# Kernel optimization log

Measured on AMD Instinct MI355X. Metric: run time of the kernel, lower is better.

The kernel has to match this reference:

```python
import jax, jax.numpy as jnp
import numpy as np

N_NODES = 100000
N_EDGES = 800000
NODE_DIM = 128
HIDDEN = 256
OUT_DIM = 512
N_LAYERS = 4
N_GRAPHS = 64


def _linear_init(key, out_f, in_f):
    kw, kb = jax.random.split(key)
    bound = 1.0 / np.sqrt(in_f)
    w = jax.random.uniform(kw, (out_f, in_f), jnp.float32, -bound, bound)
    b = jax.random.uniform(kb, (out_f,), jnp.float32, -bound, bound)
    return w, b


def setup_inputs() -> dict:
    key = jax.random.key(0)
    ks = jax.random.split(key, 16)
    x = jax.random.normal(ks[0], (N_NODES, NODE_DIM), jnp.float32)
    edge_index = jax.random.randint(ks[1], (2, N_EDGES), 0, N_NODES, jnp.int64)
    batch = jnp.sort(jax.random.randint(ks[2], (N_NODES,), 0, N_GRAPHS, jnp.int64))
    node_w, node_b = _linear_init(ks[3], HIDDEN, NODE_DIM)
    gw1, gb1, gw2, gb2 = [], [], [], []
    for i in range(N_LAYERS):
        w1, b1 = _linear_init(ks[4 + 2 * i], HIDDEN, HIDDEN)
        w2, b2 = _linear_init(ks[5 + 2 * i], HIDDEN, HIDDEN)
        gw1.append(w1); gb1.append(b1); gw2.append(w2); gb2.append(b2)
    gin_w1 = jnp.stack(gw1); gin_b1 = jnp.stack(gb1)
    gin_w2 = jnp.stack(gw2); gin_b2 = jnp.stack(gb2)
    eps = jnp.zeros((N_LAYERS,), jnp.float32)  # train_eps init 0
    out_w1, out_b1 = _linear_init(ks[12], HIDDEN, HIDDEN)
    out_w2, out_b2 = _linear_init(ks[13], OUT_DIM, HIDDEN)
    return {
        "x": x, "edge_index": edge_index, "batch": batch,
        "node_w": node_w, "node_b": node_b,
        "gin_w1": gin_w1, "gin_b1": gin_b1,
        "gin_w2": gin_w2, "gin_b2": gin_b2, "eps": eps,
        "out_w1": out_w1, "out_b1": out_b1,
        "out_w2": out_w2, "out_b2": out_b2,
    }


def reference(x, edge_index, batch, node_w, node_b, gin_w1, gin_b1, gin_w2,
              gin_b2, eps, out_w1, out_b1, out_w2, out_b2):
    src, dst = edge_index[0], edge_index[1]
    # node projection + relu
    h = jax.nn.relu(x @ node_w.T + node_b)  # [N, H]
    for i in range(N_LAYERS):
        # GINConv: mlp((1+eps)*x + sum_{j in N(i)} x_j); x_j = h[src], agg at dst
        agg = jax.ops.segment_sum(h[src], dst, num_segments=N_NODES)
        z = (1.0 + eps[i]) * h + agg
        z = jax.nn.relu(z @ gin_w1[i].T + gin_b1[i])
        z = z @ gin_w2[i].T + gin_b2[i]
        h = jax.nn.relu(z)  # outer relu in forward
    # global_mean_pool over batch assignment
    counts = jax.ops.segment_sum(jnp.ones((N_NODES,), h.dtype), batch,
                                 num_segments=N_GRAPHS)
    sums = jax.ops.segment_sum(h, batch, num_segments=N_GRAPHS)
    h_graph = sums / jnp.maximum(counts, 1.0)[:, None]  # [B, H]
    out = jax.nn.relu(h_graph @ out_w1.T + out_b1) @ out_w2.T + out_b2
    return out  # [B, OUT_DIM]
```

## Files before the change

kernel.cpp:

```cpp
#include <hip/hip_runtime.h>
#include <stdint.h>

#define N_NODES   100000
#define N_EDGES   800000
#define NODE_DIM  128
#define HIDDEN    256
#define OUT_DIM   512
#define N_LAYERS  4
#define N_GRAPHS  64
#define POOL_CHUNKS 8
#define SCAN_BLK  1024
#define SCAN_NB   ((N_NODES + SCAN_BLK - 1) / SCAN_BLK)

typedef _Float16 f16;
typedef __attribute__((ext_vector_type(8)))  _Float16 f16x8;
typedef __attribute__((ext_vector_type(4)))  _Float16 f16x4;
typedef __attribute__((ext_vector_type(4)))  float    f32x4;
typedef __attribute__((ext_vector_type(16))) float    f32x16;

__global__ void k_f2h(const float* __restrict__ in, f16* __restrict__ out, int n4) {
    int i = blockIdx.x * 256 + threadIdx.x;
    if (i < n4) {
        f32x4 v = *(const f32x4*)(in + (size_t)i * 4);
        f16x4 o;
        o[0] = (f16)v[0]; o[1] = (f16)v[1]; o[2] = (f16)v[2]; o[3] = (f16)v[3];
        *(f16x4*)(out + (size_t)i * 4) = o;
    }
}

__global__ void k_hist(const int* __restrict__ ei, int* __restrict__ deg) {
    int e = blockIdx.x * 256 + threadIdx.x;
    if (e < N_EDGES) atomicAdd(&deg[ei[N_EDGES + e]], 1);
}

__global__ __launch_bounds__(1024) void k_scan1(const int* __restrict__ deg,
                                                int* __restrict__ rowptr,
                                                int* __restrict__ bsums) {
    __shared__ int tmp[SCAN_BLK];
    int tid = threadIdx.x;
    int i = blockIdx.x * SCAN_BLK + tid;
    int v = (i < N_NODES) ? deg[i] : 0;
    tmp[tid] = v;
    __syncthreads();
    for (int off = 1; off < SCAN_BLK; off <<= 1) {
        int t = (tid >= off) ? tmp[tid - off] : 0;
        __syncthreads();
        tmp[tid] += t;
        __syncthreads();
    }
    if (i < N_NODES) rowptr[i] = tmp[tid] - v;
    if (tid == SCAN_BLK - 1) bsums[blockIdx.x] = tmp[tid];
}

__global__ __launch_bounds__(128) void k_scan2(const int* __restrict__ bsums,
                                               int* __restrict__ boffs,
                                               int* __restrict__ rowptr) {
    __shared__ int tmp[128];
    int tid = threadIdx.x;
    int v = (tid < SCAN_NB) ? bsums[tid] : 0;
    tmp[tid] = v;
    __syncthreads();
    for (int off = 1; off < 128; off <<= 1) {
        int t = (tid >= off) ? tmp[tid - off] : 0;
        __syncthreads();
        tmp[tid] += t;
        __syncthreads();
    }
    if (tid < SCAN_NB) boffs[tid] = tmp[tid] - v;
    if (tid == 127) rowptr[N_NODES] = tmp[127];
}

__global__ __launch_bounds__(1024) void k_scan3(int* __restrict__ rowptr,
                                                const int* __restrict__ boffs,
                                                int* __restrict__ cursor) {
    int i = blockIdx.x * SCAN_BLK + threadIdx.x;
    if (i < N_NODES) {
        int r = rowptr[i] + boffs[blockIdx.x];
        rowptr[i] = r;
        cursor[i] = r;
    }
}

__global__ void k_scatter(const int* __restrict__ ei, int* __restrict__ cursor,
                          int* __restrict__ col) {
    int e = blockIdx.x * 256 + threadIdx.x;
    if (e < N_EDGES) {
        int d = ei[N_EDGES + e];
        int p = atomicAdd(&cursor[d], 1);
        col[p] = ei[e];
    }
}

__global__ __launch_bounds__(256) void k_agg(const f16* __restrict__ h,
                                             const int* __restrict__ rowptr,
                                             const int* __restrict__ col,
                                             const float* __restrict__ eps, int layer,
                                             f16* __restrict__ z) {
    int node = blockIdx.x * 4 + (threadIdx.x >> 6);
    if (node >= N_NODES) return;
    int lane = threadIdx.x & 63;
    int half = lane >> 5;
    int c0 = (lane & 31) * 8;
    float e1 = 1.0f + eps[layer];
    float a0 = 0, a1 = 0, a2 = 0, a3 = 0, a4 = 0, a5 = 0, a6 = 0, a7 = 0;
    int jb = rowptr[node], je = rowptr[node + 1];
    int j = jb;
    for (; j + 8 <= je; j += 8) {
        int s0 = col[j     + half];
        int s1 = col[j + 2 + half];
        int s2 = col[j + 4 + half];
        int s3 = col[j + 6 + half];
        f16x8 v0 = *(const f16x8*)(h + (size_t)s0 * HIDDEN + c0);
        f16x8 v1 = *(const f16x8*)(h + (size_t)s1 * HIDDEN + c0);
        f16x8 v2 = *(const f16x8*)(h + (size_t)s2 * HIDDEN + c0);
        f16x8 v3 = *(const f16x8*)(h + (size_t)s3 * HIDDEN + c0);
        a0 += (float)v0[0] + (float)v1[0] + (float)v2[0] + (float)v3[0];
        a1 += (float)v0[1] + (float)v1[1] + (float)v2[1] + (float)v3[1];
        a2 += (float)v0[2] + (float)v1[2] + (float)v2[2] + (float)v3[2];
        a3 += (float)v0[3] + (float)v1[3] + (float)v2[3] + (float)v3[3];
        a4 += (float)v0[4] + (float)v1[4] + (float)v2[4] + (float)v3[4];
        a5 += (float)v0[5] + (float)v1[5] + (float)v2[5] + (float)v3[5];
        a6 += (float)v0[6] + (float)v1[6] + (float)v2[6] + (float)v3[6];
        a7 += (float)v0[7] + (float)v1[7] + (float)v2[7] + (float)v3[7];
    }
    for (; j + 2 <= je; j += 2) {
        int s = col[j + half];
        f16x8 v = *(const f16x8*)(h + (size_t)s * HIDDEN + c0);
        a0 += (float)v[0]; a1 += (float)v[1]; a2 += (float)v[2]; a3 += (float)v[3];
        a4 += (float)v[4]; a5 += (float)v[5]; a6 += (float)v[6]; a7 += (float)v[7];
    }
    if (j < je && half == 0) {
        int s = col[j];
        f16x8 v = *(const f16x8*)(h + (size_t)s * HIDDEN + c0);
        a0 += (float)v[0]; a1 += (float)v[1]; a2 += (float)v[2]; a3 += (float)v[3];
        a4 += (float)v[4]; a5 += (float)v[5]; a6 += (float)v[6]; a7 += (float)v[7];
    }
    if (half == 0) {
        f16x8 hv = *(const f16x8*)(h + (size_t)node * HIDDEN + c0);
        a0 += e1 * (float)hv[0]; a1 += e1 * (float)hv[1];
        a2 += e1 * (float)hv[2]; a3 += e1 * (float)hv[3];
        a4 += e1 * (float)hv[4]; a5 += e1 * (float)hv[5];
        a6 += e1 * (float)hv[6]; a7 += e1 * (float)hv[7];
    }
    a0 += __shfl_xor(a0, 32); a1 += __shfl_xor(a1, 32);
    a2 += __shfl_xor(a2, 32); a3 += __shfl_xor(a3, 32);
    a4 += __shfl_xor(a4, 32); a5 += __shfl_xor(a5, 32);
    a6 += __shfl_xor(a6, 32); a7 += __shfl_xor(a7, 32);
    if (half == 0) {
        f16x8 o;
        o[0] = (f16)a0; o[1] = (f16)a1; o[2] = (f16)a2; o[3] = (f16)a3;
        o[4] = (f16)a4; o[5] = (f16)a5; o[6] = (f16)a6; o[7] = (f16)a7;
        *(f16x8*)(z + (size_t)node * HIDDEN + c0) = o;
    }
}

template<int K>
__global__ __launch_bounds__(512) void k_gemm(const f16* __restrict__ A,
                                              const f16* __restrict__ B,
                                              const float* __restrict__ bias,
                                              f16* __restrict__ C, int nsl32) {
    constexpr int NPANEL = K >> 6;
    constexpr int NKS    = K >> 4;
    __shared__ f16 Bs[NPANEL * 256 * 64];
    const int tid = threadIdx.x, wid = tid >> 6, lane = tid & 63;
    const int hi  = lane >> 5;
    const int l31 = lane & 31;

#pragma unroll
    for (int p = 0; p < NPANEL; ++p) {
#pragma unroll
        for (int r = 0; r < 4; ++r) {
            int chunk = (r << 9) + tid;
            int brow = chunk >> 3, c8 = chunk & 7;
            int sc8  = c8 ^ (brow & 7);
            const f16* src = B + (size_t)brow * K + (p << 6) + sc8 * 8;
            f16* dst = Bs + (p << 14) + (size_t)((r << 9) + (wid << 6)) * 8;
            __builtin_amdgcn_global_load_lds((const __attribute__((address_space(1))) void*)src,
                                             (__attribute__((address_space(3))) void*)dst, 16, 0, 0);
        }
    }
    __syncthreads();

    for (int s = blockIdx.x * 8 + wid; s < nsl32; s += (gridDim.x << 3)) {
        const int r0 = s << 5;
        f16x8 a[NKS];
        const f16* arow = A + (size_t)(r0 + l31) * K + (hi << 3);
#pragma unroll
        for (int ks = 0; ks < NKS; ++ks)
            a[ks] = *(const f16x8*)(arow + (ks << 4));
#pragma unroll
        for (int hf = 0; hf < 2; ++hf) {
            f32x16 acc[4] = {};
#pragma unroll
            for (int ks = 0; ks < NKS; ++ks) {
                const int kk = ((ks & 3) << 1) | hi;
                const f16* pb = Bs + ((ks >> 2) << 14);
#pragma unroll
                for (int n = 0; n < 4; ++n) {
                    int rb = (hf << 7) + (n << 5) + l31;
                    f16x8 bf = *(const f16x8*)(pb + rb * 64 + ((kk ^ (rb & 7)) << 3));
                    acc[n] = __builtin_amdgcn_mfma_f32_32x32x16_f16(a[ks], bf, acc[n], 0, 0, 0);
                }
            }
#pragma unroll
            for (int n = 0; n < 4; ++n) {
                int gc = (hf << 7) + (n << 5) + l31;
                float bv = bias[gc];
#pragma unroll
                for (int reg = 0; reg < 16; ++reg) {
                    int gr = r0 + (reg & 3) + ((reg >> 2) << 3) + (hi << 2);
                    float v = fmaxf(acc[n][reg] + bv, 0.0f);
                    C[(size_t)gr * HIDDEN + gc] = (f16)v;
                }
            }
        }
    }
}

__global__ void k_bounds(const int* __restrict__ batch, int* __restrict__ starts) {
    int i = blockIdx.x * 256 + threadIdx.x;
    if (i >= N_NODES) return;
    int g  = batch[i];
    int gp = (i == 0) ? -1 : batch[i - 1];
    for (int q = gp + 1; q <= g; ++q) starts[q] = i;
    if (i == N_NODES - 1) {
        for (int q = g + 1; q <= N_GRAPHS; ++q) starts[q] = N_NODES;
    }
}

__global__ __launch_bounds__(256) void k_pool(const f16* __restrict__ h,
                                              const int* __restrict__ starts,
                                              float* __restrict__ part) {
    int g = blockIdx.x, ch = blockIdx.y, c = threadIdx.x;
    int s = starts[g], e = starts[g + 1];
    int len = e - s;
    int per = (len + POOL_CHUNKS - 1) / POOL_CHUNKS;
    int lo = s + ch * per;
    int hi = lo + per; if (hi > e) hi = e;
    float acc = 0.0f;
    for (int n = lo; n < hi; ++n) acc += (float)h[(size_t)n * HIDDEN + c];
    part[((size_t)g * POOL_CHUNKS + ch) * HIDDEN + c] = acc;
}

__global__ __launch_bounds__(256) void k_head(const float* __restrict__ part,
                                              const int* __restrict__ starts,
                                              const float* __restrict__ w1,
                                              const float* __restrict__ b1,
                                              const float* __restrict__ w2,
                                              const float* __restrict__ b2,
                                              float* __restrict__ out) {
    __shared__ float hg[HIDDEN];
    __shared__ float t[HIDDEN];
    int g = blockIdx.x, tid = threadIdx.x;
    int cnti = starts[g + 1] - starts[g];
    float cnt = (float)(cnti > 1 ? cnti : 1);
    float s = 0.0f;
#pragma unroll
    for (int ch = 0; ch < POOL_CHUNKS; ++ch)
        s += part[((size_t)g * POOL_CHUNKS + ch) * HIDDEN + tid];
    hg[tid] = s / cnt;
    __syncthreads();
    float a = b1[tid];
    for (int k = 0; k < HIDDEN; ++k) a += hg[k] * w1[(size_t)tid * HIDDEN + k];
    t[tid] = fmaxf(a, 0.0f);
    __syncthreads();
    for (int j = tid; j < OUT_DIM; j += 256) {
        float o = b2[j];
        for (int k = 0; k < HIDDEN; ++k) o += t[k] * w2[(size_t)j * HIDDEN + k];
        out[(size_t)g * OUT_DIM + j] = o;
    }
}

extern "C" void kernel_launch(void* const* d_in, const int* in_sizes, int n_in,
                              void* d_out, int out_size, void* d_ws, size_t ws_size,
                              hipStream_t stream) {
    const float* x      = (const float*)d_in[0];
    const int*   ei     = (const int*)d_in[1];
    const int*   batch  = (const int*)d_in[2];
    const float* node_w = (const float*)d_in[3];
    const float* node_b = (const float*)d_in[4];
    const float* gw1    = (const float*)d_in[5];
    const float* gb1    = (const float*)d_in[6];
    const float* gw2    = (const float*)d_in[7];
    const float* gb2    = (const float*)d_in[8];
    const float* eps    = (const float*)d_in[9];
    const float* ow1    = (const float*)d_in[10];
    const float* ob1    = (const float*)d_in[11];
    const float* ow2    = (const float*)d_in[12];
    const float* ob2    = (const float*)d_in[13];
    float* out = (float*)d_out;

    char* p = (char*)d_ws;
    auto alloc = [&](size_t bytes) {
        char* r = p;
        p += (bytes + 255) & ~(size_t)255;
        return (void*)r;
    };
    f16* hb   = (f16*)alloc((size_t)N_NODES * HIDDEN * 2);
    f16* zb   = (f16*)alloc((size_t)N_NODES * HIDDEN * 2);
    f16* tb   = (f16*)alloc((size_t)N_NODES * HIDDEN * 2);
    f16* xb   = (f16*)alloc((size_t)N_NODES * NODE_DIM * 2);
    f16* nwb  = (f16*)alloc((size_t)HIDDEN * NODE_DIM * 2);
    f16* w1b  = (f16*)alloc((size_t)N_LAYERS * HIDDEN * HIDDEN * 2);
    f16* w2b  = (f16*)alloc((size_t)N_LAYERS * HIDDEN * HIDDEN * 2);
    int* deg    = (int*)alloc((size_t)N_NODES * 4);
    int* rowptr = (int*)alloc((size_t)(N_NODES + 1) * 4);
    int* cursor = (int*)alloc((size_t)N_NODES * 4);
    int* col    = (int*)alloc((size_t)N_EDGES * 4);
    float* part = (float*)alloc((size_t)N_GRAPHS * POOL_CHUNKS * HIDDEN * 4);
    int* starts = (int*)alloc((size_t)(N_GRAPHS + 1) * 4);
    int* bsums  = (int*)alloc((size_t)SCAN_NB * 4);
    int* boffs  = (int*)alloc((size_t)SCAN_NB * 4);
    (void)in_sizes; (void)n_in; (void)out_size; (void)ws_size;

    hipMemsetAsync(deg, 0, (size_t)N_NODES * 4, stream);

    k_f2h<<<(N_NODES * NODE_DIM / 4 + 255) / 256, 256, 0, stream>>>(x, xb, N_NODES * NODE_DIM / 4);
    k_f2h<<<(HIDDEN * NODE_DIM / 4 + 255) / 256, 256, 0, stream>>>(node_w, nwb, HIDDEN * NODE_DIM / 4);
    k_f2h<<<(N_LAYERS * HIDDEN * HIDDEN / 4 + 255) / 256, 256, 0, stream>>>(gw1, w1b, N_LAYERS * HIDDEN * HIDDEN / 4);
    k_f2h<<<(N_LAYERS * HIDDEN * HIDDEN / 4 + 255) / 256, 256, 0, stream>>>(gw2, w2b, N_LAYERS * HIDDEN * HIDDEN / 4);

    k_hist<<<(N_EDGES + 255) / 256, 256, 0, stream>>>(ei, deg);
    k_scan1<<<SCAN_NB, SCAN_BLK, 0, stream>>>(deg, rowptr, bsums);
    k_scan2<<<1, 128, 0, stream>>>(bsums, boffs, rowptr);
    k_scan3<<<SCAN_NB, SCAN_BLK, 0, stream>>>(rowptr, boffs, cursor);
    k_scatter<<<(N_EDGES + 255) / 256, 256, 0, stream>>>(ei, cursor, col);

    k_bounds<<<(N_NODES + 255) / 256, 256, 0, stream>>>(batch, starts);

    const int NSL32 = N_NODES / 32;
    k_gemm<NODE_DIM><<<256, 512, 0, stream>>>(xb, nwb, node_b, hb, NSL32);

    for (int l = 0; l < N_LAYERS; ++l) {
        k_agg<<<(N_NODES + 3) / 4, 256, 0, stream>>>(hb, rowptr, col, eps, l, zb);
        k_gemm<HIDDEN><<<256, 512, 0, stream>>>(zb, w1b + (size_t)l * HIDDEN * HIDDEN,
                                                gb1 + (size_t)l * HIDDEN, tb, NSL32);
        k_gemm<HIDDEN><<<256, 512, 0, stream>>>(tb, w2b + (size_t)l * HIDDEN * HIDDEN,
                                                gb2 + (size_t)l * HIDDEN, hb, NSL32);
    }

    dim3 pgrid(N_GRAPHS, POOL_CHUNKS);
    k_pool<<<pgrid, 256, 0, stream>>>(hb, starts, part);
    k_head<<<N_GRAPHS, 256, 0, stream>>>(part, starts, ow1, ob1, ow2, ob2, out);
}
```

Before: 697.9 us.

## Tile aggregation by 32-column feature slices across 32 nodes per block

```diff
diff --git a/kernel.cpp b/kernel.cpp
--- a/kernel.cpp
+++ b/kernel.cpp
@@ -96,62 +96,34 @@
                                              const int* __restrict__ col,
                                              const float* __restrict__ eps, int layer,
                                              f16* __restrict__ z) {
-    int node = blockIdx.x * 4 + (threadIdx.x >> 6);
-    if (node >= N_NODES) return;
-    int lane = threadIdx.x & 63;
-    int half = lane >> 5;
-    int c0 = (lane & 31) * 8;
-    float e1 = 1.0f + eps[layer];
-    float a0 = 0, a1 = 0, a2 = 0, a3 = 0, a4 = 0, a5 = 0, a6 = 0, a7 = 0;
+    const int node = blockIdx.y * 32 + (threadIdx.x >> 3);
+    const int c0 = (blockIdx.x << 5) + ((threadIdx.x & 7) << 2);
+    const float e1 = 1.0f + eps[layer];
+    const f16* hc = h + c0;
+    f16x4 hv = *(const f16x4*)(hc + (size_t)node * HIDDEN);
+    float a0 = e1 * (float)hv[0], a1 = e1 * (float)hv[1];
+    float a2 = e1 * (float)hv[2], a3 = e1 * (float)hv[3];
     int jb = rowptr[node], je = rowptr[node + 1];
     int j = jb;
-    for (; j + 8 <= je; j += 8) {
-        int s0 = col[j     + half];
-        int s1 = col[j + 2 + half];
-        int s2 = col[j + 4 + half];
-        int s3 = col[j + 6 + half];
-        f16x8 v0 = *(const f16x8*)(h + (size_t)s0 * HIDDEN + c0);
-        f16x8 v1 = *(const f16x8*)(h + (size_t)s1 * HIDDEN + c0);
-        f16x8 v2 = *(const f16x8*)(h + (size_t)s2 * HIDDEN + c0);
-        f16x8 v3 = *(const f16x8*)(h + (size_t)s3 * HIDDEN + c0);
+    for (; j + 4 <= je; j += 4) {
+        int s0 = col[j], s1 = col[j + 1], s2 = col[j + 2], s3 = col[j + 3];
+        f16x4 v0 = *(const f16x4*)(hc + (size_t)s0 * HIDDEN);
+        f16x4 v1 = *(const f16x4*)(hc + (size_t)s1 * HIDDEN);
+        f16x4 v2 = *(const f16x4*)(hc + (size_t)s2 * HIDDEN);
+        f16x4 v3 = *(const f16x4*)(hc + (size_t)s3 * HIDDEN);
         a0 += (float)v0[0] + (float)v1[0] + (float)v2[0] + (float)v3[0];
         a1 += (float)v0[1] + (float)v1[1] + (float)v2[1] + (float)v3[1];
         a2 += (float)v0[2] + (float)v1[2] + (float)v2[2] + (float)v3[2];
         a3 += (float)v0[3] + (float)v1[3] + (float)v2[3] + (float)v3[3];
-        a4 += (float)v0[4] + (float)v1[4] + (float)v2[4] + (float)v3[4];
-        a5 += (float)v0[5] + (float)v1[5] + (float)v2[5] + (float)v3[5];
-        a6 += (float)v0[6] + (float)v1[6] + (float)v2[6] + (float)v3[6];
-        a7 += (float)v0[7] + (float)v1[7] + (float)v2[7] + (float)v3[7];
-    }
-    for (; j + 2 <= je; j += 2) {
-        int s = col[j + half];
-        f16x8 v = *(const f16x8*)(h + (size_t)s * HIDDEN + c0);
+    }
+    for (; j < je; ++j) {
+        int s = col[j];
+        f16x4 v = *(const f16x4*)(hc + (size_t)s * HIDDEN);
         a0 += (float)v[0]; a1 += (float)v[1]; a2 += (float)v[2]; a3 += (float)v[3];
-        a4 += (float)v[4]; a5 += (float)v[5]; a6 += (float)v[6]; a7 += (float)v[7];
-    }
-    if (j < je && half == 0) {
-        int s = col[j];
-        f16x8 v = *(const f16x8*)(h + (size_t)s * HIDDEN + c0);
-        a0 += (float)v[0]; a1 += (float)v[1]; a2 += (float)v[2]; a3 += (float)v[3];
-        a4 += (float)v[4]; a5 += (float)v[5]; a6 += (float)v[6]; a7 += (float)v[7];
-    }
-    if (half == 0) {
-        f16x8 hv = *(const f16x8*)(h + (size_t)node * HIDDEN + c0);
-        a0 += e1 * (float)hv[0]; a1 += e1 * (float)hv[1];
-        a2 += e1 * (float)hv[2]; a3 += e1 * (float)hv[3];
-        a4 += e1 * (float)hv[4]; a5 += e1 * (float)hv[5];
-        a6 += e1 * (float)hv[6]; a7 += e1 * (float)hv[7];
-    }
-    a0 += __shfl_xor(a0, 32); a1 += __shfl_xor(a1, 32);
-    a2 += __shfl_xor(a2, 32); a3 += __shfl_xor(a3, 32);
-    a4 += __shfl_xor(a4, 32); a5 += __shfl_xor(a5, 32);
-    a6 += __shfl_xor(a6, 32); a7 += __shfl_xor(a7, 32);
-    if (half == 0) {
-        f16x8 o;
-        o[0] = (f16)a0; o[1] = (f16)a1; o[2] = (f16)a2; o[3] = (f16)a3;
-        o[4] = (f16)a4; o[5] = (f16)a5; o[6] = (f16)a6; o[7] = (f16)a7;
-        *(f16x8*)(z + (size_t)node * HIDDEN + c0) = o;
-    }
+    }
+    f16x4 o;
+    o[0] = (f16)a0; o[1] = (f16)a1; o[2] = (f16)a2; o[3] = (f16)a3;
+    *(f16x4*)(z + (size_t)node * HIDDEN + c0) = o;
 }
 
 template<int K>
@@ -331,8 +303,9 @@
     const int NSL32 = N_NODES / 32;
     k_gemm<NODE_DIM><<<256, 512, 0, stream>>>(xb, nwb, node_b, hb, NSL32);
 
+    dim3 agrid(8, N_NODES / 32);
     for (int l = 0; l < N_LAYERS; ++l) {
-        k_agg<<<(N_NODES + 3) / 4, 256, 0, stream>>>(hb, rowptr, col, eps, l, zb);
+        k_agg<<<agrid, 256, 0, stream>>>(hb, rowptr, col, eps, l, zb);
         k_gemm<HIDDEN><<<256, 512, 0, stream>>>(zb, w1b + (size_t)l * HIDDEN * HIDDEN,
                                                 gb1 + (size_t)l * HIDDEN, tb, NSL32);
         k_gemm<HIDDEN><<<256, 512, 0, stream>>>(tb, w2b + (size_t)l * HIDDEN * HIDDEN,
```

New measurement: 869.0 us. +24.5%, slower.
